# Performance work log

Hardware: AMD Instinct MI355X
Metric: run time of the kernel (lower is better)

The kernel has to match this reference:

```python
import jax, jax.numpy as jnp
import numpy as np

B, N, E = 4, 256, 512  # batch, max_sentence_len, embedding_size


def setup_inputs() -> dict:
    key = jax.random.key(0)
    k1, k2, k3 = jax.random.split(key, 3)
    inputs = jax.random.normal(k1, (B, N, E), dtype=jnp.float32)
    scale = 1.0 / np.sqrt(N)
    queries_weight = jax.random.normal(k2, (N, N), dtype=jnp.float32) * scale
    keys_weight = jax.random.normal(k3, (N, N), dtype=jnp.float32) * scale
    return {"inputs": inputs, "queries_weight": queries_weight, "keys_weight": keys_weight}


def reference(inputs, queries_weight, keys_weight):
    # Original math: for each position i, weights are masked to the top-left
    # (i+1)x(i+1) block:  QW[i,n,p] = Qw[n,p]*(n<=i)*(p<=i)  (same for keys).
    # queries[b,i,m,p] = sum_{n<=i} x[b,n,m] Qw[n,p] * (p<=i)  -> cumsum over n.
    # keys[b,i,p,q]    = sum_{n<=i} x[b,n,q] Kw[n,p] * (p<=i)
    # attn[b,i,m,q] = sum_p queries[b,i,m,p] keys[b,i,p,q]
    # fit[b,i,m]    = sum_q attn[b,i,m,q] x[b,i,q]
    #               = sum_p queries[b,i,m,p] * (sum_q keys[b,i,p,q] x[b,i,q])
    # The (p<=i) mask appears squared, so applying it once suffices.
    b, n, e = inputs.shape
    tri = jnp.tril(jnp.ones((n, n), dtype=inputs.dtype))  # tri[i,p] = (p <= i)

    # (B,N,E,N): cumulative (over source position) outer products
    Qcum = jnp.cumsum(jnp.einsum('bnm,np->bnmp', inputs, queries_weight), axis=1)
    Qcum = Qcum * tri[None, :, None, :]
    Kcum = jnp.cumsum(jnp.einsum('bnq,np->bnqp', inputs, keys_weight), axis=1)

    s = jnp.einsum('biqp,biq->bip', Kcum, inputs)      # keys contracted with x_i
    fitnesses = jnp.einsum('bimp,bip->bim', Qcum, s)   # (B,N,E)
    avg_fitness = jnp.einsum('bim,bim->bi', inputs, fitnesses)[..., None]
    net_fitnesses = fitnesses - avg_fitness
    return inputs + inputs * net_fitnesses
```

## Files before the change

kernel.cpp:

```cpp
#include <hip/hip_runtime.h>

#define B_ 4
#define N_ 256
#define E_ 512


__global__ __launch_bounds__(256) void prep_kernel(
    const float* __restrict__ X, const float* __restrict__ Qw,
    float* __restrict__ QwT, float* __restrict__ Gpart) {

    const int bx = blockIdx.x, by = blockIdx.y, bz = blockIdx.z;
    const int tx = threadIdx.x, ty = threadIdx.y;
    const int tid = ty * 16 + tx;

    if (bz == 16) {
        __shared__ float tt[64][68];
        const int r = tid >> 2, c0 = tid & 3;
#pragma unroll
        for (int cc = 0; cc < 4; ++cc) {
            const int c = (c0 + cc * 4) * 4;
            const float4 v = *(const float4*)&Qw[(by * 64 + r) * N_ + bx * 64 + c];
            tt[c + 0][r] = v.x; tt[c + 1][r] = v.y;
            tt[c + 2][r] = v.z; tt[c + 3][r] = v.w;
        }
        __syncthreads();
#pragma unroll
        for (int cc = 0; cc < 4; ++cc) {
            const int c = (c0 + cc * 4) * 4;
            const float4 v = *(const float4*)&tt[r][c];
            *(float4*)&QwT[(bx * 64 + r) * N_ + by * 64 + c] = v;
        }
        return;
    }

    const int b = bz >> 2, kq = bz & 3;
    const float* __restrict__ Xb = X + (size_t)b * N_ * E_;
    __shared__ float At[32][68];
    __shared__ float Bt[32][68];
    float acc[4][4] = {};
    const int r = tid >> 2, c0 = tid & 3;

    for (int k0 = kq * 128; k0 < kq * 128 + 128; k0 += 32) {
        {
            const float4 va = *(const float4*)&Xb[(size_t)(by * 64 + r) * E_ + k0 + c0 * 8];
            const float4 vb = *(const float4*)&Xb[(size_t)(by * 64 + r) * E_ + k0 + c0 * 8 + 4];
            At[c0*8+0][r] = va.x; At[c0*8+1][r] = va.y; At[c0*8+2][r] = va.z; At[c0*8+3][r] = va.w;
            At[c0*8+4][r] = vb.x; At[c0*8+5][r] = vb.y; At[c0*8+6][r] = vb.z; At[c0*8+7][r] = vb.w;
            const float4 wa = *(const float4*)&Xb[(size_t)(bx * 64 + r) * E_ + k0 + c0 * 8];
            const float4 wb = *(const float4*)&Xb[(size_t)(bx * 64 + r) * E_ + k0 + c0 * 8 + 4];
            Bt[c0*8+0][r] = wa.x; Bt[c0*8+1][r] = wa.y; Bt[c0*8+2][r] = wa.z; Bt[c0*8+3][r] = wa.w;
            Bt[c0*8+4][r] = wb.x; Bt[c0*8+5][r] = wb.y; Bt[c0*8+6][r] = wb.z; Bt[c0*8+7][r] = wb.w;
        }
        __syncthreads();
#pragma unroll
        for (int kk = 0; kk < 32; ++kk) {
            const float4 a  = *(const float4*)&At[kk][ty * 4];
            const float4 bb = *(const float4*)&Bt[kk][tx * 4];
            acc[0][0] += a.x*bb.x; acc[0][1] += a.x*bb.y; acc[0][2] += a.x*bb.z; acc[0][3] += a.x*bb.w;
            acc[1][0] += a.y*bb.x; acc[1][1] += a.y*bb.y; acc[1][2] += a.y*bb.z; acc[1][3] += a.y*bb.w;
            acc[2][0] += a.z*bb.x; acc[2][1] += a.z*bb.y; acc[2][2] += a.z*bb.z; acc[2][3] += a.z*bb.w;
            acc[3][0] += a.w*bb.x; acc[3][1] += a.w*bb.y; acc[3][2] += a.w*bb.z; acc[3][3] += a.w*bb.w;
        }
        __syncthreads();
    }
    float* gout = Gpart + ((size_t)(kq * 4 + b) * N_ + by * 64 + ty * 4) * N_ + bx * 64 + tx * 4;
#pragma unroll
    for (int qi = 0; qi < 4; ++qi)
        *(float4*)&gout[(size_t)qi * N_] =
            make_float4(acc[qi][0], acc[qi][1], acc[qi][2], acc[qi][3]);
}

__device__ __forceinline__ void fma4(float4& a, float c, const float4& v) {
    a.x += c * v.x; a.y += c * v.y; a.z += c * v.z; a.w += c * v.w;
}

__global__ __launch_bounds__(256) void fused_kernel(
    const float* __restrict__ X, const float* __restrict__ Kw,
    const float* __restrict__ QwT, const float* __restrict__ Gpart,
    float* __restrict__ out) {

    const int blk = blockIdx.x;
    const int b   = blk >> 8;
    const int j   = blk & 255;
    const int i   = (b & 1) ? (255 - j) : j;

    const int tid  = threadIdx.x;
    const int lane = tid & 63, wid = tid >> 6;

    const float4* __restrict__ Xb4 = (const float4*)(X + (size_t)b * N_ * E_);
    const float4* __restrict__ Kw4 = (const float4*)Kw;
    const float4* __restrict__ Qt4 = (const float4*)QwT;

    __shared__ float  xi[E_];
    __shared__ float  gv[N_];
    __shared__ float  sv[N_];
    __shared__ float  tv[N_];
    __shared__ float4 sp[4][128];
    __shared__ float  avgv;
    __shared__ float  red[4];
    float* const spf = (float*)sp;

    if (tid < 128) ((float4*)xi)[tid] = Xb4[(size_t)i * 128 + tid];
    {
        float s = 0.f;
#pragma unroll
        for (int q = 0; q < 4; ++q)
            s += Gpart[((size_t)(q * 4 + b) * N_ + i) * N_ + tid];
        gv[tid] = (tid <= i) ? s : 0.f;
    }
    __syncthreads();

    const int Mc  = (i + 32) & ~31;
    const int cnt = Mc >> 2;
    const int nb  = wid * cnt;

    {
        float4 a0 = {0,0,0,0};
        for (int t8 = 0; t8 < cnt; t8 += 8) {
            const int n0 = nb + t8;
#pragma unroll
            for (int u = 0; u < 8; ++u)
                fma4(a0, gv[n0 + u], Kw4[(size_t)(n0 + u) * 64 + lane]);
        }
        sp[wid][lane] = a0;
    }
    __syncthreads();
    sv[tid] = (tid <= i)
        ? (spf[0*512 + tid] + spf[1*512 + tid] + spf[2*512 + tid] + spf[3*512 + tid])
        : 0.f;
    __syncthreads();

    {
        float4 a0 = {0,0,0,0};
        for (int t8 = 0; t8 < cnt; t8 += 8) {
            const int p0 = nb + t8;
#pragma unroll
            for (int u = 0; u < 8; ++u)
                fma4(a0, sv[p0 + u], Qt4[(size_t)(p0 + u) * 64 + lane]);
        }
        sp[wid][lane] = a0;
    }
    __syncthreads();
    tv[tid] = (tid <= i)
        ? (spf[0*512 + tid] + spf[1*512 + tid] + spf[2*512 + tid] + spf[3*512 + tid])
        : 0.f;
    __syncthreads();

    {
        float v = tv[tid] * gv[tid];
#pragma unroll
        for (int off = 32; off > 0; off >>= 1)
            v += __shfl_xor(v, off, 64);
        if (lane == 0) red[wid] = v;
        __syncthreads();
        if (tid == 0) avgv = red[0] + red[1] + red[2] + red[3];
    }
    __syncthreads();

    {
        float4 f0 = {0,0,0,0}, f1 = {0,0,0,0};
        for (int t8 = 0; t8 < cnt; t8 += 8) {
            const int n0 = nb + t8;
#pragma unroll
            for (int u = 0; u < 8; ++u) {
                const float tc = tv[n0 + u];
                fma4(f0, tc, Xb4[(size_t)(n0 + u) * 128 + lane]);
                fma4(f1, tc, Xb4[(size_t)(n0 + u) * 128 + 64 + lane]);
            }
        }
        sp[wid][lane]      = f0;
        sp[wid][64 + lane] = f1;
    }
    __syncthreads();
    {
        const float a0 = avgv;
        float* const o = out + ((size_t)b * N_ + i) * E_;
        const float fit0 = spf[0*512 + tid]       + spf[1*512 + tid]
                         + spf[2*512 + tid]       + spf[3*512 + tid];
        const float fit1 = spf[0*512 + 256 + tid] + spf[1*512 + 256 + tid]
                         + spf[2*512 + 256 + tid] + spf[3*512 + 256 + tid];
        o[tid]       = xi[tid]       * (1.f + fit0 - a0);
        o[tid + 256] = xi[tid + 256] * (1.f + fit1 - a0);
    }
}

extern "C" void kernel_launch(void* const* d_in, const int* in_sizes, int n_in,
                              void* d_out, int out_size, void* d_ws, size_t ws_size,
                              hipStream_t stream) {
    const float* X  = (const float*)d_in[0];
    const float* Qw = (const float*)d_in[1];
    const float* Kw = (const float*)d_in[2];
    float* out = (float*)d_out;

    float* QwT   = (float*)d_ws;
    float* Gpart = QwT + (size_t)N_ * N_;

    prep_kernel<<<dim3(4, 4, 17), dim3(16, 16), 0, stream>>>(X, Qw, QwT, Gpart);
    fused_kernel<<<B_ * N_, 256, 0, stream>>>(X, Kw, QwT, Gpart, out);
}
```

Baseline: 88.96 us.

## Process four output rows per block to reuse Kw, QwT and X loads

Each block of the fused kernel now handles four rows i (two low and two mirrored high rows, to balance the triangular work) with 512 threads instead of one row with 256. Each Kw, QwT and X vector loaded from global memory is reused across four accumulators, cutting global and L2 traffic per row by roughly four times. In exchange the block count drops from 1024 to 256, so occupancy and parallelism fall. Shared memory use grows to about 32KB of partial sums, and the loop length is set by the largest of the four rows, which may do some wasted work.

Measured after the change: 82.60 us. 7.2% less time.

```diff
diff --git a/kernel.cpp b/kernel.cpp
--- a/kernel.cpp
+++ b/kernel.cpp
@@ -74,15 +74,18 @@
     a.x += c * v.x; a.y += c * v.y; a.z += c * v.z; a.w += c * v.w;
 }
 
-__global__ __launch_bounds__(256) void fused_kernel(
+__global__ __launch_bounds__(512) void fused_kernel(
     const float* __restrict__ X, const float* __restrict__ Kw,
     const float* __restrict__ QwT, const float* __restrict__ Gpart,
     float* __restrict__ out) {
 
     const int blk = blockIdx.x;
-    const int b   = blk >> 8;
-    const int j   = blk & 255;
-    const int i   = (b & 1) ? (255 - j) : j;
+    const int b   = blk >> 6;
+    const int j   = blk & 63;
+    int irow[4];
+    irow[0] = 2 * j;     irow[1] = 2 * j + 1;
+    irow[2] = 254 - 2*j; irow[3] = 255 - 2*j;
+    const int maxi = irow[3] > irow[1] ? irow[3] : irow[1];
 
     const int tid  = threadIdx.x;
     const int lane = tid & 63, wid = tid >> 6;
@@ -91,96 +94,158 @@
     const float4* __restrict__ Kw4 = (const float4*)Kw;
     const float4* __restrict__ Qt4 = (const float4*)QwT;
 
-    __shared__ float  xi[E_];
-    __shared__ float  gv[N_];
-    __shared__ float  sv[N_];
-    __shared__ float  tv[N_];
-    __shared__ float4 sp[4][128];
-    __shared__ float  avgv;
-    __shared__ float  red[4];
-    float* const spf = (float*)sp;
-
-    if (tid < 128) ((float4*)xi)[tid] = Xb4[(size_t)i * 128 + tid];
-    {
-        float s = 0.f;
-#pragma unroll
-        for (int q = 0; q < 4; ++q)
-            s += Gpart[((size_t)(q * 4 + b) * N_ + i) * N_ + tid];
-        gv[tid] = (tid <= i) ? s : 0.f;
-    }
-    __syncthreads();
-
-    const int Mc  = (i + 32) & ~31;
-    const int cnt = Mc >> 2;
+    __shared__ float  xi[4][E_];
+    __shared__ float  gT[N_][4];
+    __shared__ float  sT[N_][4];
+    __shared__ float  tT[N_][4];
+    __shared__ float4 sp4[2048];
+    __shared__ float  avgv[4];
+    __shared__ float  red[4][4];
+    float* const spf = (float*)sp4;
+
+    {
+        const int r = tid >> 7, c = tid & 127;
+        ((float4*)xi[r])[c] = Xb4[(size_t)irow[r] * 128 + c];
+    }
+    if (tid < N_) {
+#pragma unroll
+        for (int r = 0; r < 4; ++r) {
+            float s = 0.f;
+#pragma unroll
+            for (int q = 0; q < 4; ++q)
+                s += Gpart[((size_t)(q * 4 + b) * N_ + irow[r]) * N_ + tid];
+            gT[tid][r] = (tid <= irow[r]) ? s : 0.f;
+        }
+    }
+    __syncthreads();
+
+    const int Mc  = (maxi + 32) & ~31;
+    const int cnt = Mc >> 3;
     const int nb  = wid * cnt;
 
     {
-        float4 a0 = {0,0,0,0};
-        for (int t8 = 0; t8 < cnt; t8 += 8) {
-            const int n0 = nb + t8;
-#pragma unroll
-            for (int u = 0; u < 8; ++u)
-                fma4(a0, gv[n0 + u], Kw4[(size_t)(n0 + u) * 64 + lane]);
-        }
-        sp[wid][lane] = a0;
-    }
-    __syncthreads();
-    sv[tid] = (tid <= i)
-        ? (spf[0*512 + tid] + spf[1*512 + tid] + spf[2*512 + tid] + spf[3*512 + tid])
-        : 0.f;
-    __syncthreads();
-
-    {
-        float4 a0 = {0,0,0,0};
-        for (int t8 = 0; t8 < cnt; t8 += 8) {
-            const int p0 = nb + t8;
-#pragma unroll
-            for (int u = 0; u < 8; ++u)
-                fma4(a0, sv[p0 + u], Qt4[(size_t)(p0 + u) * 64 + lane]);
-        }
-        sp[wid][lane] = a0;
-    }
-    __syncthreads();
-    tv[tid] = (tid <= i)
-        ? (spf[0*512 + tid] + spf[1*512 + tid] + spf[2*512 + tid] + spf[3*512 + tid])
-        : 0.f;
-    __syncthreads();
-
-    {
-        float v = tv[tid] * gv[tid];
-#pragma unroll
-        for (int off = 32; off > 0; off >>= 1)
-            v += __shfl_xor(v, off, 64);
-        if (lane == 0) red[wid] = v;
-        __syncthreads();
-        if (tid == 0) avgv = red[0] + red[1] + red[2] + red[3];
-    }
-    __syncthreads();
-
-    {
-        float4 f0 = {0,0,0,0}, f1 = {0,0,0,0};
-        for (int t8 = 0; t8 < cnt; t8 += 8) {
-            const int n0 = nb + t8;
-#pragma unroll
-            for (int u = 0; u < 8; ++u) {
-                const float tc = tv[n0 + u];
-                fma4(f0, tc, Xb4[(size_t)(n0 + u) * 128 + lane]);
-                fma4(f1, tc, Xb4[(size_t)(n0 + u) * 128 + 64 + lane]);
+        float4 a[4] = {{0,0,0,0},{0,0,0,0},{0,0,0,0},{0,0,0,0}};
+        for (int t4 = 0; t4 < cnt; t4 += 4) {
+#pragma unroll
+            for (int u = 0; u < 4; ++u) {
+                const int n = nb + t4 + u;
+                const float4 kv = Kw4[(size_t)n * 64 + lane];
+                const float4 gp = *(const float4*)&gT[n][0];
+                fma4(a[0], gp.x, kv); fma4(a[1], gp.y, kv);
+                fma4(a[2], gp.z, kv); fma4(a[3], gp.w, kv);
             }
         }
-        sp[wid][lane]      = f0;
-        sp[wid][64 + lane] = f1;
-    }
-    __syncthreads();
-    {
-        const float a0 = avgv;
-        float* const o = out + ((size_t)b * N_ + i) * E_;
-        const float fit0 = spf[0*512 + tid]       + spf[1*512 + tid]
-                         + spf[2*512 + tid]       + spf[3*512 + tid];
-        const float fit1 = spf[0*512 + 256 + tid] + spf[1*512 + 256 + tid]
-                         + spf[2*512 + 256 + tid] + spf[3*512 + 256 + tid];
-        o[tid]       = xi[tid]       * (1.f + fit0 - a0);
-        o[tid + 256] = xi[tid + 256] * (1.f + fit1 - a0);
+#pragma unroll
+        for (int r = 0; r < 4; ++r)
+            sp4[(wid * 4 + r) * 64 + lane] = a[r];
+    }
+    __syncthreads();
+    {
+        const int p = tid & 255, rbase = (tid >> 8) * 2;
+#pragma unroll
+        for (int rr = 0; rr < 2; ++rr) {
+            const int r = rbase + rr;
+            float v = 0.f;
+#pragma unroll
+            for (int w = 0; w < 8; ++w)
+                v += spf[(w * 4 + r) * 256 + p];
+            sT[p][r] = (p <= irow[r]) ? v : 0.f;
+        }
+    }
+    __syncthreads();
+
+    {
+        float4 a[4] = {{0,0,0,0},{0,0,0,0},{0,0,0,0},{0,0,0,0}};
+        for (int t4 = 0; t4 < cnt; t4 += 4) {
+#pragma unroll
+            for (int u = 0; u < 4; ++u) {
+                const int p = nb + t4 + u;
+                const float4 qv = Qt4[(size_t)p * 64 + lane];
+                const float4 sv = *(const float4*)&sT[p][0];
+                fma4(a[0], sv.x, qv); fma4(a[1], sv.y, qv);
+                fma4(a[2], sv.z, qv); fma4(a[3], sv.w, qv);
+            }
+        }
+#pragma unroll
+        for (int r = 0; r < 4; ++r)
+            sp4[(wid * 4 + r) * 64 + lane] = a[r];
+    }
+    __syncthreads();
+    {
+        const int p = tid & 255, rbase = (tid >> 8) * 2;
+#pragma unroll
+        for (int rr = 0; rr < 2; ++rr) {
+            const int r = rbase + rr;
+            float v = 0.f;
+#pragma unroll
+            for (int w = 0; w < 8; ++w)
+                v += spf[(w * 4 + r) * 256 + p];
+            tT[p][r] = (p <= irow[r]) ? v : 0.f;
+        }
+    }
+    __syncthreads();
+
+    if (tid < N_) {
+        float v0 = tT[tid][0] * gT[tid][0];
+        float v1 = tT[tid][1] * gT[tid][1];
+        float v2 = tT[tid][2] * gT[tid][2];
+        float v3 = tT[tid][3] * gT[tid][3];
+#pragma unroll
+        for (int off = 32; off > 0; off >>= 1) {
+            v0 += __shfl_xor(v0, off, 64);
+            v1 += __shfl_xor(v1, off, 64);
+            v2 += __shfl_xor(v2, off, 64);
+            v3 += __shfl_xor(v3, off, 64);
+        }
+        if (lane == 0) {
+            red[wid][0] = v0; red[wid][1] = v1;
+            red[wid][2] = v2; red[wid][3] = v3;
+        }
+    }
+    __syncthreads();
+    if (tid == 0) {
+#pragma unroll
+        for (int r = 0; r < 4; ++r)
+            avgv[r] = red[0][r] + red[1][r] + red[2][r] + red[3][r];
+    }
+    __syncthreads();
+
+    float4 f[4][2] = {{{0,0,0,0},{0,0,0,0}},{{0,0,0,0},{0,0,0,0}},
+                      {{0,0,0,0},{0,0,0,0}},{{0,0,0,0},{0,0,0,0}}};
+    {
+        for (int t2 = 0; t2 < cnt; t2 += 2) {
+#pragma unroll
+            for (int u = 0; u < 2; ++u) {
+                const int n = nb + t2 + u;
+                const float4 xa = Xb4[(size_t)n * 128 + lane];
+                const float4 xb = Xb4[(size_t)n * 128 + 64 + lane];
+                const float4 tv = *(const float4*)&tT[n][0];
+                fma4(f[0][0], tv.x, xa); fma4(f[0][1], tv.x, xb);
+                fma4(f[1][0], tv.y, xa); fma4(f[1][1], tv.y, xb);
+                fma4(f[2][0], tv.z, xa); fma4(f[2][1], tv.z, xb);
+                fma4(f[3][0], tv.w, xa); fma4(f[3][1], tv.w, xb);
+            }
+        }
+    }
+#pragma unroll
+    for (int h = 0; h < 2; ++h) {
+        __syncthreads();
+#pragma unroll
+        for (int rr = 0; rr < 2; ++rr) {
+            sp4[(wid * 2 + rr) * 128 + lane]      = f[2 * h + rr][0];
+            sp4[(wid * 2 + rr) * 128 + 64 + lane] = f[2 * h + rr][1];
+        }
+        __syncthreads();
+#pragma unroll
+        for (int rr = 0; rr < 2; ++rr) {
+            const int r = 2 * h + rr;
+            float fit = 0.f;
+#pragma unroll
+            for (int w = 0; w < 8; ++w)
+                fit += spf[(w * 2 + rr) * 512 + tid];
+            float* const o = out + ((size_t)b * N_ + irow[r]) * E_;
+            o[tid] = xi[r][tid] * (1.f + fit - avgv[r]);
+        }
     }
 }
 
@@ -196,5 +261,5 @@
     float* Gpart = QwT + (size_t)N_ * N_;
 
     prep_kernel<<<dim3(4, 4, 17), dim3(16, 16), 0, stream>>>(X, Qw, QwT, Gpart);
-    fused_kernel<<<B_ * N_, 256, 0, stream>>>(X, Kw, QwT, Gpart, out);
-}
+    fused_kernel<<<B_ * (N_ / 4), 512, 0, stream>>>(X, Kw, QwT, Gpart, out);
+}
```

## Replace per-row fused kernel with batched triangular tiled GEMM kernels

Applied to the files above, without the earlier changes.

The per-position fused kernel, which did three matrix-vector passes for each row i, is replaced by three block-tiled GEMM kernels (S = G·Kw, T = S·QwT, out = T·X). These kernels exploit the lower-triangular masking to skip tiles, and split-K partial sums go to workspace. The goal is reuse of weight and X tiles across 64 rows instead of re-streaming them per row. In exchange there are two extra kernel launches, more global-memory traffic for the partial-sum buffers, and partial sums reduced redundantly in the consumer kernels.

New measurement: 100.5 us. 12.9% more time.

```diff
diff --git a/kernel.cpp b/kernel.cpp
--- a/kernel.cpp
+++ b/kernel.cpp
@@ -4,6 +4,9 @@
 #define N_ 256
 #define E_ 512
 
+#define OFF_GP 65536
+#define OFF_SP 1114112
+#define OFF_TP 2162688
 
 __global__ __launch_bounds__(256) void prep_kernel(
     const float* __restrict__ X, const float* __restrict__ Qw,
@@ -70,117 +73,232 @@
             make_float4(acc[qi][0], acc[qi][1], acc[qi][2], acc[qi][3]);
 }
 
-__device__ __forceinline__ void fma4(float4& a, float c, const float4& v) {
-    a.x += c * v.x; a.y += c * v.y; a.z += c * v.z; a.w += c * v.w;
-}
-
-__global__ __launch_bounds__(256) void fused_kernel(
-    const float* __restrict__ X, const float* __restrict__ Kw,
-    const float* __restrict__ QwT, const float* __restrict__ Gpart,
+__global__ __launch_bounds__(256) void sgemm_kernel(
+    const float* __restrict__ Kw, float* __restrict__ ws) {
+
+    const int pt = blockIdx.x, it = blockIdx.y;
+    const int b  = blockIdx.z >> 2, kq = blockIdx.z & 3;
+    if (pt > it || kq > it) return;
+
+    const float* __restrict__ Gpart = ws + OFF_GP;
+    float* __restrict__ Spart = ws + OFF_SP;
+
+    const int tx = threadIdx.x, ty = threadIdx.y;
+    const int tid = ty * 16 + tx;
+
+    __shared__ float At[64][68];
+    __shared__ float Bt[64][68];
+
+    {
+        const int i_loc = tid >> 2, c0 = tid & 3;
+        float av[16];
+#pragma unroll
+        for (int e = 0; e < 16; ++e) av[e] = 0.f;
+#pragma unroll
+        for (int q = 0; q < 4; ++q) {
+            const float* src = Gpart + ((size_t)(q * 4 + b) * N_ + it * 64 + i_loc) * N_
+                             + kq * 64 + c0 * 16;
+#pragma unroll
+            for (int v = 0; v < 4; ++v) {
+                const float4 f = *(const float4*)&src[v * 4];
+                av[v*4+0] += f.x; av[v*4+1] += f.y; av[v*4+2] += f.z; av[v*4+3] += f.w;
+            }
+        }
+        if (kq == it) {
+#pragma unroll
+            for (int e = 0; e < 16; ++e)
+                if (c0 * 16 + e > i_loc) av[e] = 0.f;
+        }
+#pragma unroll
+        for (int e = 0; e < 16; ++e) At[c0 * 16 + e][i_loc] = av[e];
+    }
+    {
+        const int k = tid >> 2, c0 = tid & 3;
+        const float* src = Kw + (size_t)(kq * 64 + k) * N_ + pt * 64 + c0 * 16;
+#pragma unroll
+        for (int v = 0; v < 4; ++v)
+            *(float4*)&Bt[k][c0 * 16 + v * 4] = *(const float4*)&src[v * 4];
+    }
+    __syncthreads();
+
+    float acc[4][4] = {};
+#pragma unroll 8
+    for (int kk = 0; kk < 64; ++kk) {
+        const float4 a  = *(const float4*)&At[kk][ty * 4];
+        const float4 bb = *(const float4*)&Bt[kk][tx * 4];
+        acc[0][0] += a.x*bb.x; acc[0][1] += a.x*bb.y; acc[0][2] += a.x*bb.z; acc[0][3] += a.x*bb.w;
+        acc[1][0] += a.y*bb.x; acc[1][1] += a.y*bb.y; acc[1][2] += a.y*bb.z; acc[1][3] += a.y*bb.w;
+        acc[2][0] += a.z*bb.x; acc[2][1] += a.z*bb.y; acc[2][2] += a.z*bb.z; acc[2][3] += a.z*bb.w;
+        acc[3][0] += a.w*bb.x; acc[3][1] += a.w*bb.y; acc[3][2] += a.w*bb.z; acc[3][3] += a.w*bb.w;
+    }
+
+    float* sout = Spart + ((size_t)(kq * 4 + b) * N_ + it * 64 + ty * 4) * N_ + pt * 64 + tx * 4;
+#pragma unroll
+    for (int ri = 0; ri < 4; ++ri)
+        *(float4*)&sout[(size_t)ri * N_] =
+            make_float4(acc[ri][0], acc[ri][1], acc[ri][2], acc[ri][3]);
+}
+
+__global__ __launch_bounds__(256) void tgemm_kernel(
+    const float* __restrict__ ws_c, float* __restrict__ ws) {
+
+    const int nt = blockIdx.x, it = blockIdx.y;
+    const int b  = blockIdx.z >> 2, kp = blockIdx.z & 3;
+    if (nt > it || kp > it) return;
+
+    const float* __restrict__ QwT   = ws_c;
+    const float* __restrict__ Spart = ws_c + OFF_SP;
+    float* __restrict__ Tpart = ws + OFF_TP;
+
+    const int tx = threadIdx.x, ty = threadIdx.y;
+    const int tid = ty * 16 + tx;
+
+    __shared__ float At[64][68];
+    __shared__ float Bt[64][68];
+
+    {
+        const int i_loc = tid >> 2, c0 = tid & 3;
+        float av[16];
+#pragma unroll
+        for (int e = 0; e < 16; ++e) av[e] = 0.f;
+        for (int q = 0; q <= it; ++q) {
+            const float* src = Spart + ((size_t)(q * 4 + b) * N_ + it * 64 + i_loc) * N_
+                             + kp * 64 + c0 * 16;
+#pragma unroll
+            for (int v = 0; v < 4; ++v) {
+                const float4 f = *(const float4*)&src[v * 4];
+                av[v*4+0] += f.x; av[v*4+1] += f.y; av[v*4+2] += f.z; av[v*4+3] += f.w;
+            }
+        }
+        if (kp == it) {
+#pragma unroll
+            for (int e = 0; e < 16; ++e)
+                if (c0 * 16 + e > i_loc) av[e] = 0.f;
+        }
+#pragma unroll
+        for (int e = 0; e < 16; ++e) At[c0 * 16 + e][i_loc] = av[e];
+    }
+    {
+        const int k = tid >> 2, c0 = tid & 3;
+        const float* src = QwT + (size_t)(kp * 64 + k) * N_ + nt * 64 + c0 * 16;
+#pragma unroll
+        for (int v = 0; v < 4; ++v)
+            *(float4*)&Bt[k][c0 * 16 + v * 4] = *(const float4*)&src[v * 4];
+    }
+    __syncthreads();
+
+    float acc[4][4] = {};
+#pragma unroll 8
+    for (int kk = 0; kk < 64; ++kk) {
+        const float4 a  = *(const float4*)&At[kk][ty * 4];
+        const float4 bb = *(const float4*)&Bt[kk][tx * 4];
+        acc[0][0] += a.x*bb.x; acc[0][1] += a.x*bb.y; acc[0][2] += a.x*bb.z; acc[0][3] += a.x*bb.w;
+        acc[1][0] += a.y*bb.x; acc[1][1] += a.y*bb.y; acc[1][2] += a.y*bb.z; acc[1][3] += a.y*bb.w;
+        acc[2][0] += a.z*bb.x; acc[2][1] += a.z*bb.y; acc[2][2] += a.z*bb.z; acc[2][3] += a.z*bb.w;
+        acc[3][0] += a.w*bb.x; acc[3][1] += a.w*bb.y; acc[3][2] += a.w*bb.z; acc[3][3] += a.w*bb.w;
+    }
+
+    float* tout = Tpart + ((size_t)(kp * 4 + b) * N_ + it * 64 + ty * 4) * N_ + nt * 64 + tx * 4;
+#pragma unroll
+    for (int ri = 0; ri < 4; ++ri)
+        *(float4*)&tout[(size_t)ri * N_] =
+            make_float4(acc[ri][0], acc[ri][1], acc[ri][2], acc[ri][3]);
+}
+
+__global__ __launch_bounds__(256) void final_kernel(
+    const float* __restrict__ X, const float* __restrict__ ws_c,
     float* __restrict__ out) {
 
-    const int blk = blockIdx.x;
-    const int b   = blk >> 8;
-    const int j   = blk & 255;
-    const int i   = (b & 1) ? (255 - j) : j;
-
-    const int tid  = threadIdx.x;
-    const int lane = tid & 63, wid = tid >> 6;
-
-    const float4* __restrict__ Xb4 = (const float4*)(X + (size_t)b * N_ * E_);
-    const float4* __restrict__ Kw4 = (const float4*)Kw;
-    const float4* __restrict__ Qt4 = (const float4*)QwT;
-
-    __shared__ float  xi[E_];
-    __shared__ float  gv[N_];
-    __shared__ float  sv[N_];
-    __shared__ float  tv[N_];
-    __shared__ float4 sp[4][128];
-    __shared__ float  avgv;
-    __shared__ float  red[4];
-    float* const spf = (float*)sp;
-
-    if (tid < 128) ((float4*)xi)[tid] = Xb4[(size_t)i * 128 + tid];
-    {
-        float s = 0.f;
-#pragma unroll
-        for (int q = 0; q < 4; ++q)
-            s += Gpart[((size_t)(q * 4 + b) * N_ + i) * N_ + tid];
-        gv[tid] = (tid <= i) ? s : 0.f;
-    }
+    const int mt = blockIdx.x, rt = blockIdx.y, b = blockIdx.z;
+    const int it_eff = rt >> 1;
+    const int ibase  = (rt & 1) * 32;
+
+    const float* __restrict__ Gpart = ws_c + OFF_GP;
+    const float* __restrict__ Tpart = ws_c + OFF_TP;
+    const float* __restrict__ Xb = X + (size_t)b * N_ * E_;
+
+    const int tx = threadIdx.x, ty = threadIdx.y;
+    const int tid = ty * 16 + tx;
+
+    __shared__ float At[64][36];
+    __shared__ float Bt[64][68];
+    __shared__ float avr[32][9];
+
+    float acc[2][4] = {};
+    float avgacc = 0.f;
+
+    for (int kn = 0; kn <= it_eff; ++kn) {
+        {
+            const int r = tid >> 3, c0 = tid & 7;
+            float tvv[8], gvv[8];
+#pragma unroll
+            for (int e = 0; e < 8; ++e) { tvv[e] = 0.f; gvv[e] = 0.f; }
+            for (int q = 0; q <= it_eff; ++q) {
+                const float* src = Tpart + ((size_t)(q * 4 + b) * N_ + rt * 32 + r) * N_
+                                 + kn * 64 + c0 * 8;
+#pragma unroll
+                for (int v = 0; v < 2; ++v) {
+                    const float4 f = *(const float4*)&src[v * 4];
+                    tvv[v*4+0] += f.x; tvv[v*4+1] += f.y; tvv[v*4+2] += f.z; tvv[v*4+3] += f.w;
+                }
+            }
+#pragma unroll
+            for (int q = 0; q < 4; ++q) {
+                const float* src = Gpart + ((size_t)(q * 4 + b) * N_ + rt * 32 + r) * N_
+                                 + kn * 64 + c0 * 8;
+#pragma unroll
+                for (int v = 0; v < 2; ++v) {
+                    const float4 f = *(const float4*)&src[v * 4];
+                    gvv[v*4+0] += f.x; gvv[v*4+1] += f.y; gvv[v*4+2] += f.z; gvv[v*4+3] += f.w;
+                }
+            }
+            if (kn == it_eff) {
+#pragma unroll
+                for (int e = 0; e < 8; ++e)
+                    if (c0 * 8 + e > ibase + r) tvv[e] = 0.f;
+            }
+#pragma unroll
+            for (int e = 0; e < 8; ++e) {
+                avgacc += tvv[e] * gvv[e];
+                At[c0 * 8 + e][r] = tvv[e];
+            }
+        }
+        {
+            const int k = tid >> 2, c0 = tid & 3;
+            const float* src = Xb + (size_t)(kn * 64 + k) * E_ + mt * 64 + c0 * 16;
+#pragma unroll
+            for (int v = 0; v < 4; ++v)
+                *(float4*)&Bt[k][c0 * 16 + v * 4] = *(const float4*)&src[v * 4];
+        }
+        __syncthreads();
+
+#pragma unroll 8
+        for (int kk = 0; kk < 64; ++kk) {
+            const float2 a  = *(const float2*)&At[kk][ty * 2];
+            const float4 bb = *(const float4*)&Bt[kk][tx * 4];
+            acc[0][0] += a.x*bb.x; acc[0][1] += a.x*bb.y; acc[0][2] += a.x*bb.z; acc[0][3] += a.x*bb.w;
+            acc[1][0] += a.y*bb.x; acc[1][1] += a.y*bb.y; acc[1][2] += a.y*bb.z; acc[1][3] += a.y*bb.w;
+        }
+        __syncthreads();
+    }
+
+    avr[tid >> 3][tid & 7] = avgacc;
     __syncthreads();
 
-    const int Mc  = (i + 32) & ~31;
-    const int cnt = Mc >> 2;
-    const int nb  = wid * cnt;
-
-    {
-        float4 a0 = {0,0,0,0};
-        for (int t8 = 0; t8 < cnt; t8 += 8) {
-            const int n0 = nb + t8;
-#pragma unroll
-            for (int u = 0; u < 8; ++u)
-                fma4(a0, gv[n0 + u], Kw4[(size_t)(n0 + u) * 64 + lane]);
-        }
-        sp[wid][lane] = a0;
-    }
-    __syncthreads();
-    sv[tid] = (tid <= i)
-        ? (spf[0*512 + tid] + spf[1*512 + tid] + spf[2*512 + tid] + spf[3*512 + tid])
-        : 0.f;
-    __syncthreads();
-
-    {
-        float4 a0 = {0,0,0,0};
-        for (int t8 = 0; t8 < cnt; t8 += 8) {
-            const int p0 = nb + t8;
-#pragma unroll
-            for (int u = 0; u < 8; ++u)
-                fma4(a0, sv[p0 + u], Qt4[(size_t)(p0 + u) * 64 + lane]);
-        }
-        sp[wid][lane] = a0;
-    }
-    __syncthreads();
-    tv[tid] = (tid <= i)
-        ? (spf[0*512 + tid] + spf[1*512 + tid] + spf[2*512 + tid] + spf[3*512 + tid])
-        : 0.f;
-    __syncthreads();
-
-    {
-        float v = tv[tid] * gv[tid];
-#pragma unroll
-        for (int off = 32; off > 0; off >>= 1)
-            v += __shfl_xor(v, off, 64);
-        if (lane == 0) red[wid] = v;
-        __syncthreads();
-        if (tid == 0) avgv = red[0] + red[1] + red[2] + red[3];
-    }
-    __syncthreads();
-
-    {
-        float4 f0 = {0,0,0,0}, f1 = {0,0,0,0};
-        for (int t8 = 0; t8 < cnt; t8 += 8) {
-            const int n0 = nb + t8;
-#pragma unroll
-            for (int u = 0; u < 8; ++u) {
-                const float tc = tv[n0 + u];
-                fma4(f0, tc, Xb4[(size_t)(n0 + u) * 128 + lane]);
-                fma4(f1, tc, Xb4[(size_t)(n0 + u) * 128 + 64 + lane]);
-            }
-        }
-        sp[wid][lane]      = f0;
-        sp[wid][64 + lane] = f1;
-    }
-    __syncthreads();
-    {
-        const float a0 = avgv;
-        float* const o = out + ((size_t)b * N_ + i) * E_;
-        const float fit0 = spf[0*512 + tid]       + spf[1*512 + tid]
-                         + spf[2*512 + tid]       + spf[3*512 + tid];
-        const float fit1 = spf[0*512 + 256 + tid] + spf[1*512 + 256 + tid]
-                         + spf[2*512 + 256 + tid] + spf[3*512 + 256 + tid];
-        o[tid]       = xi[tid]       * (1.f + fit0 - a0);
-        o[tid + 256] = xi[tid + 256] * (1.f + fit1 - a0);
+#pragma unroll
+    for (int ri = 0; ri < 2; ++ri) {
+        const int row = ty * 2 + ri;
+        float avg = 0.f;
+#pragma unroll
+        for (int c = 0; c < 8; ++c) avg += avr[row][c];
+        const int gi = rt * 32 + row;
+        const float4 xv = *(const float4*)&Xb[(size_t)gi * E_ + mt * 64 + tx * 4];
+        float4 ov;
+        ov.x = xv.x * (1.f + acc[ri][0] - avg);
+        ov.y = xv.y * (1.f + acc[ri][1] - avg);
+        ov.z = xv.z * (1.f + acc[ri][2] - avg);
+        ov.w = xv.w * (1.f + acc[ri][3] - avg);
+        *(float4*)&out[((size_t)b * N_ + gi) * E_ + mt * 64 + tx * 4] = ov;
     }
 }
 
@@ -191,10 +309,13 @@
     const float* Qw = (const float*)d_in[1];
     const float* Kw = (const float*)d_in[2];
     float* out = (float*)d_out;
-
-    float* QwT   = (float*)d_ws;
-    float* Gpart = QwT + (size_t)N_ * N_;
-
-    prep_kernel<<<dim3(4, 4, 17), dim3(16, 16), 0, stream>>>(X, Qw, QwT, Gpart);
-    fused_kernel<<<B_ * N_, 256, 0, stream>>>(X, Kw, QwT, Gpart, out);
-}
+    float* ws  = (float*)d_ws;
+
+    float* QwT   = ws;
+    float* Gpart = ws + OFF_GP;
+
+    prep_kernel <<<dim3(4, 4, 17), dim3(16, 16), 0, stream>>>(X, Qw, QwT, Gpart);
+    sgemm_kernel<<<dim3(4, 4, 16), dim3(16, 16), 0, stream>>>(Kw, ws);
+    tgemm_kernel<<<dim3(4, 4, 16), dim3(16, 16), 0, stream>>>(ws, ws);
+    final_kernel<<<dim3(8, 8, 4),  dim3(16, 16), 0, stream>>>(X, ws, out);
+}
```
